# Performance work log

Measured on AMD Instinct MI355X. Metric: run time of the kernel, lower is better.

Reference implementation:

```python
import jax, jax.numpy as jnp
import numpy as np

B, NKV, NQ, D, H = 4, 2048, 1024, 1024, 16
HD = D // H


def setup_inputs() -> dict:
    key = jax.random.key(0)
    ks = jax.random.split(key, 9)
    s = 0.02
    return {
        "x": jax.random.normal(ks[0], (B, NKV, D), jnp.float32),
        "y": jax.random.normal(ks[1], (B, NQ, D), jnp.float32),
        "mask": jax.random.randint(ks[2], (B, NQ, NKV), 0, 2, jnp.int32),
        "W_kv": jax.random.normal(ks[3], (D, 2 * D), jnp.float32) * s,
        "b_kv": jnp.zeros((2 * D,), jnp.float32),
        "W_q": jax.random.normal(ks[4], (D, D), jnp.float32) * s,
        "b_q": jnp.zeros((D,), jnp.float32),
        "W_o": jax.random.normal(ks[5], (D, D), jnp.float32) * s,
        "b_o": jnp.zeros((D,), jnp.float32),
    }


def reference(x, y, mask, W_kv, b_kv, W_q, b_q, W_o, b_o):
    b, nkv, _ = x.shape
    nq = y.shape[1]
    kv = x @ W_kv + b_kv                                  # [B, NKV, 2D]
    q = y @ W_q + b_q                                     # [B, NQ, D]
    kv = kv.reshape(b, nkv, H, 2 * HD).transpose(0, 2, 1, 3)  # [B,H,NKV,2HD]
    q = q.reshape(b, nq, H, HD).transpose(0, 2, 1, 3)         # [B,H,NQ,HD]
    k, v = kv[..., :HD], kv[..., HD:]
    scores = jnp.einsum('bhqd,bhkd->bhqk', q, k) / jnp.sqrt(jnp.float32(HD))
    scores = jnp.where(mask[:, None, :, :] == 0, jnp.float32(-1e20), scores)
    attn = jax.nn.softmax(scores, axis=-1)
    vals = jnp.einsum('bhqk,bhkd->bhqd', attn, v)          # [B,H,NQ,HD]
    vals = vals.transpose(0, 2, 1, 3).reshape(b, nq, D)
    return vals @ W_o + b_o
```

## Files before the change

### kernel.cpp

```cpp
#include <hip/hip_runtime.h>
#include <hip/hip_bf16.h>
#include <math.h>

#define B_   4
#define NKV_ 2048
#define NQ_  1024
#define D_   1024
#define H_   16
#define HD_  64

typedef __attribute__((ext_vector_type(8))) short bf16x8;
typedef __attribute__((ext_vector_type(4))) float f32x4;

#define MFMA16x32(a, b, c) __builtin_amdgcn_mfma_f32_16x16x32_bf16((a), (b), (c), 0, 0, 0)

#define SC_LOG2 0.1803368801111244f

__device__ __forceinline__ short f2bf(float f) {
    unsigned u = __builtin_bit_cast(unsigned, f);
    u = (u + 0x7fff + ((u >> 16) & 1)) >> 16;
    return (short)u;
}
__device__ __forceinline__ unsigned cvt_pk_bf16(float lo, float hi) {
    unsigned r;
    asm("v_cvt_pk_bf16_f32 %0, %1, %2" : "=v"(r) : "v"(lo), "v"(hi));
    return r;
}
__device__ __forceinline__ void gload_lds16(const void* g, void* l) {
    __builtin_amdgcn_global_load_lds(
        (const __attribute__((address_space(1))) void*)g,
        (__attribute__((address_space(3))) void*)l, 16, 0, 0);
}
__device__ __forceinline__ void barrier_raw() {
    asm volatile("" ::: "memory");
    __builtin_amdgcn_s_barrier();
    asm volatile("" ::: "memory");
}

__global__ __launch_bounds__(256)
void prep(const float* __restrict__ Wkv, short* __restrict__ Tkv,
          const float* __restrict__ Wq,  short* __restrict__ Tq,
          const float* __restrict__ Wo,  short* __restrict__ To,
          const int* __restrict__ mask,  unsigned short* __restrict__ m16,
          const float* __restrict__ x,   short* __restrict__ xh, int n4x,
          const float* __restrict__ y,   short* __restrict__ yh, int n4y)
{
    const int bid = (int)blockIdx.x;
    if (bid < 4096) {
        const float* W; short* T; int K, N, bx, by;
        if (bid < 2048)      { W = Wkv; T = Tkv; K = D_; N = 2 * D_; bx = bid & 63;          by = bid >> 6; }
        else if (bid < 3072) { W = Wq;  T = Tq;  K = D_; N = D_;     bx = (bid - 2048) & 31; by = (bid - 2048) >> 5; }
        else                 { W = Wo;  T = To;  K = D_; N = D_;     bx = (bid - 3072) & 31; by = (bid - 3072) >> 5; }
        __shared__ float tile[32][33];
        const int tx = threadIdx.x & 31, ty = threadIdx.x >> 5;
        const int n0 = bx * 32, k0 = by * 32;
#pragma unroll
        for (int i = 0; i < 4; ++i)
            tile[ty + 8 * i][tx] = W[(size_t)(k0 + ty + 8 * i) * N + n0 + tx];
        __syncthreads();
#pragma unroll
        for (int i = 0; i < 4; ++i)
            T[(size_t)(n0 + ty + 8 * i) * K + k0 + tx] = f2bf(tile[tx][ty + 8 * i]);
    } else if (bid < 4608) {
        const int w = (bid - 4096) * 256 + threadIdx.x;
        const int4* pp = reinterpret_cast<const int4*>(mask + (size_t)w * 64);
        unsigned wg0 = 0, wg1 = 0, wg2 = 0, wg3 = 0;
#pragma unroll
        for (int i = 0; i < 16; ++i) {
            const int4 v = pp[i];
            const unsigned nib = (unsigned)(v.x != 0) | ((unsigned)(v.y != 0) << 1)
                               | ((unsigned)(v.z != 0) << 2) | ((unsigned)(v.w != 0) << 3);
            const unsigned sh = 4u * (unsigned)(i >> 2);
            if ((i & 3) == 0) wg0 |= nib << sh;
            else if ((i & 3) == 1) wg1 |= nib << sh;
            else if ((i & 3) == 2) wg2 |= nib << sh;
            else wg3 |= nib << sh;
        }
        ushort4 o;
        o.x = (unsigned short)wg0; o.y = (unsigned short)wg1;
        o.z = (unsigned short)wg2; o.w = (unsigned short)wg3;
        reinterpret_cast<ushort4*>(m16)[w] = o;
    } else {
        const int ntot = n4x + n4y;
        for (int i = (bid - 4608) * 256 + threadIdx.x; i < ntot; i += 2048 * 256) {
            const float4 v = (i < n4x)
                ? reinterpret_cast<const float4*>(x)[i]
                : reinterpret_cast<const float4*>(y)[i - n4x];
            short4 h;
            h.x = f2bf(v.x); h.y = f2bf(v.y); h.z = f2bf(v.z); h.w = f2bf(v.w);
            if (i < n4x) reinterpret_cast<short4*>(xh)[i] = h;
            else         reinterpret_cast<short4*>(yh)[i - n4x] = h;
        }
    }
}

__global__ __launch_bounds__(512, 2)
void proj256(const short* __restrict__ A, const short* __restrict__ Bm,
             const float* __restrict__ bias, short* __restrict__ Kout,
             short* __restrict__ Vtout)
{
    constexpr int K  = 1024;
    constexpr int NT = K / 32;
    constexpr int M  = B_ * NKV_;
    constexpr int N  = 2 * D_;

    __shared__ short At[4][8192];
    __shared__ short Bt[4][8192];

    const int t    = threadIdx.x;
    const int wave = t >> 6;
    const int lane = t & 63;
    const int fr   = lane & 15;
    const int kq   = lane >> 4;
    const int wm0  = (wave >> 2) * 128;
    const int wn0  = (wave & 3) * 64;

    const int gx  = N >> 8;
    const int gy  = M >> 8;
    const int lgx = __builtin_ctz(gx);
    const int bid = (int)blockIdx.x;
    const int xcd = bid & 7;
    const int j   = bid >> 3;
    const int m0  = (xcd * (gy >> 3) + (j >> lgx)) * 256;
    const int n0  = (j & (gx - 1)) * 256;

    const int r1 = t >> 2;
    const int g1 = (t & 3) ^ ((r1 >> 1) & 3);
    const int r2 = r1 + 128;

    f32x4 acc[8][4];
#pragma unroll
    for (int i = 0; i < 8; ++i)
#pragma unroll
        for (int j2 = 0; j2 < 4; ++j2) acc[i][j2] = f32x4{0.f, 0.f, 0.f, 0.f};

    auto stage = [&](int sb, int it) {
        const int kk = it << 5;
        gload_lds16(A  + (size_t)(m0 + r1) * K + kk + 8 * g1, &At[sb][wave * 512]);
        gload_lds16(A  + (size_t)(m0 + r2) * K + kk + 8 * g1, &At[sb][4096 + wave * 512]);
        gload_lds16(Bm + (size_t)(n0 + r1) * K + kk + 8 * g1, &Bt[sb][wave * 512]);
        gload_lds16(Bm + (size_t)(n0 + r2) * K + kk + 8 * g1, &Bt[sb][4096 + wave * 512]);
    };

    stage(0, 0);
    stage(1, 1);
    stage(2, 2);

    const int gsw = ((kq ^ ((fr >> 1) & 3)) << 3);
    for (int it = 0; it < NT; ++it) {
        if (it < NT - 2)       asm volatile("s_waitcnt vmcnt(8)" ::: "memory");
        else if (it == NT - 2) asm volatile("s_waitcnt vmcnt(4)" ::: "memory");
        else                   asm volatile("s_waitcnt vmcnt(0)" ::: "memory");
        barrier_raw();

        const int cb = it & 3;
        bf16x8 af[8], bf[4];
#pragma unroll
        for (int i = 0; i < 8; ++i)
            af[i] = *reinterpret_cast<const bf16x8*>(
                &At[cb][(wm0 + i * 16 + fr) * 32 + gsw]);
#pragma unroll
        for (int i = 0; i < 4; ++i)
            bf[i] = *reinterpret_cast<const bf16x8*>(
                &Bt[cb][(wn0 + i * 16 + fr) * 32 + gsw]);

        if (it + 3 < NT) stage((it + 3) & 3, it + 3);

        __builtin_amdgcn_s_setprio(1);
#pragma unroll
        for (int i = 0; i < 8; ++i)
#pragma unroll
            for (int j2 = 0; j2 < 4; ++j2)
                acc[i][j2] = MFMA16x32(af[i], bf[j2], acc[i][j2]);
        __builtin_amdgcn_s_setprio(0);
    }

#pragma unroll
    for (int i = 0; i < 8; ++i) {
#pragma unroll
        for (int j2 = 0; j2 < 4; ++j2) {
#pragma unroll
            for (int r = 0; r < 4; ++r) {
                const int m = m0 + wm0 + i * 16 + (lane >> 4) * 4 + r;
                const int n = n0 + wn0 + j2 * 16 + fr;
                const float v = acc[i][j2][r] + bias[n];
                const int b  = m >> 11;
                const int nk = m & 2047;
                const int h  = n >> 7;
                const int c  = n & 127;
                const int bh = b * H_ + h;
                if (c < 64)
                    Kout[(((size_t)bh * NKV_ + nk) << 6) + c] = f2bf(v);
                else
                    Vtout[((size_t)bh * 64 + (c - 64)) * NKV_ + nk] = f2bf(v);
            }
        }
    }
}

template<int MODE>
__global__ __launch_bounds__(256)
void gemm64(const short* __restrict__ Ahi, const short* __restrict__ Bhi,
            const float* __restrict__ bias, void* __restrict__ outv)
{
    __shared__ short At[3][2048];
    __shared__ short Bt[3][4096];

    const int M = B_ * NQ_, N = D_, K = D_;
    const int t    = threadIdx.x;
    const int wave = t >> 6;
    const int lane = t & 63;
    const int fr   = lane & 15;
    const int kq   = lane >> 4;

    const int gx  = N >> 7;
    const int gy  = M >> 6;
    const int lgx = __builtin_ctz(gx);
    const int bid = (int)blockIdx.x;
    const int xcd = bid & 7;
    const int j   = bid >> 3;
    const int m0  = (xcd * (gy >> 3) + (j >> lgx)) * 64;
    const int n0  = (j & (gx - 1)) * 128;

    const int wm0 = (wave & 1) * 32;
    const int wn0 = (wave >> 1) * 64;
    const int NT  = K >> 5;

    const int rA = t >> 2, gA = (t & 3) ^ ((rA >> 1) & 3);
    const int r1 = t >> 2,         g1 = (t & 3) ^ ((r1 >> 1) & 3);
    const int r2 = (t + 256) >> 2, g2 = (t & 3) ^ ((r2 >> 1) & 3);

    f32x4 acc[2][4];
#pragma unroll
    for (int i = 0; i < 2; ++i)
#pragma unroll
        for (int j2 = 0; j2 < 4; ++j2) acc[i][j2] = f32x4{0.f, 0.f, 0.f, 0.f};

    auto stage = [&](int sb, int it) {
        const int kk = it << 5;
        gload_lds16(Ahi + (size_t)(m0 + rA) * K + kk + 8 * gA, &At[sb][wave * 512]);
        gload_lds16(Bhi + (size_t)(n0 + r1) * K + kk + 8 * g1, &Bt[sb][wave * 512]);
        gload_lds16(Bhi + (size_t)(n0 + r2) * K + kk + 8 * g2, &Bt[sb][2048 + wave * 512]);
    };

    stage(0, 0);
    if (NT > 1) stage(1, 1);

    const int gsw = ((kq ^ ((fr >> 1) & 3)) << 3);
    for (int it = 0; it < NT; ++it) {
        if (it + 1 < NT) asm volatile("s_waitcnt vmcnt(3)" ::: "memory");
        else             asm volatile("s_waitcnt vmcnt(0)" ::: "memory");
        barrier_raw();

        const int cb = it % 3;
        bf16x8 af[2], bf[4];
#pragma unroll
        for (int i = 0; i < 2; ++i)
            af[i] = *reinterpret_cast<const bf16x8*>(&At[cb][(wm0 + i * 16 + fr) * 32 + gsw]);
#pragma unroll
        for (int i = 0; i < 4; ++i)
            bf[i] = *reinterpret_cast<const bf16x8*>(&Bt[cb][(wn0 + i * 16 + fr) * 32 + gsw]);
        if (it + 2 < NT) stage((it + 2) % 3, it + 2);

        __builtin_amdgcn_s_setprio(1);
#pragma unroll
        for (int i = 0; i < 2; ++i)
#pragma unroll
            for (int j2 = 0; j2 < 4; ++j2)
                acc[i][j2] = MFMA16x32(af[i], bf[j2], acc[i][j2]);
        __builtin_amdgcn_s_setprio(0);
    }

#pragma unroll
    for (int i = 0; i < 2; ++i)
#pragma unroll
        for (int j2 = 0; j2 < 4; ++j2)
#pragma unroll
            for (int r = 0; r < 4; ++r) {
                const int m = m0 + wm0 + i * 16 + (lane >> 4) * 4 + r;
                const int n = n0 + wn0 + j2 * 16 + fr;
                const float v = acc[i][j2][r] + bias[n];
                if (MODE == 1) {
                    short* Q_ = (short*)outv;
                    const int b = m >> 10;
                    const int q = m & 1023;
                    const int h = n >> 6;
                    const int d = n & 63;
                    Q_[(((size_t)(b * H_ + h) * NQ_ + q) << 6) + d] =
                        f2bf(v * SC_LOG2);
                } else {
                    ((float*)outv)[(size_t)m * N + n] = v;
                }
            }
}

__global__ __launch_bounds__(512)
void attn_mfma(const short* __restrict__ Q, const short* __restrict__ K,
               const short* __restrict__ Vt,
               const unsigned short* __restrict__ m16,
               short* __restrict__ valshi)
{
    __shared__ short KtL[3][4096];
    __shared__ short VtL[3][4096];
    __shared__ short PsL[8192];

    const int t    = threadIdx.x;
    const int wave = t >> 6;
    const int lane = t & 63;
    const int fr   = lane & 15;
    const int g    = lane >> 4;

    const int bid = (int)blockIdx.x;
    const int xcd = bid & 7;
    const int j   = bid >> 3;
    const int bh  = xcd * 8 + (j >> 3);
    const int b   = bh >> 4;
    const int h   = bh & 15;
    const int wq0 = (j & 7) * 128 + wave * 16;

    const short* Kg  = K  + (size_t)bh * NKV_ * 64;
    const short* Vtg = Vt + (size_t)bh * 64 * NKV_;

    bf16x8 qf0, qf1;
    {
        const short* Qg = Q + ((size_t)bh * NQ_ + wq0 + fr) * 64 + g * 8;
        qf0 = *reinterpret_cast<const bf16x8*>(Qg);
        qf1 = *reinterpret_cast<const bf16x8*>(Qg + 32);
    }

    bf16x8 ones;
#pragma unroll
    for (int i = 0; i < 8; ++i) ones[i] = (short)0x3F80;

    f32x4 acc_o[4];
#pragma unroll
    for (int n = 0; n < 4; ++n) acc_o[n] = f32x4{0.f, 0.f, 0.f, 0.f};
    f32x4 lacc = f32x4{0.f, 0.f, 0.f, 0.f};

    const unsigned short* mbp =
        m16 + ((size_t)b * NQ_ + wq0 + fr) * (NKV_ / 64) * 4 + g;

    const int r8   = lane >> 3;
    const int csw  = ((lane & 7) << 3) ^ (r8 << 3);
    const int swzf = (fr & 7) << 3;
    short* PsW = PsL + wave * (16 * 64);

    auto stage = [&](int sb, int kt) {
        const short* sK = Kg + (size_t)(kt * 64 + wave * 8 + r8) * 64 + csw;
        gload_lds16(sK, &KtL[sb][(wave * 8) * 64]);
        const short* sV = Vtg + (size_t)(wave * 8 + r8) * NKV_ + kt * 64 + csw;
        gload_lds16(sV, &VtL[sb][(wave * 8) * 64]);
    };

    constexpr int NTK = NKV_ / 64;
    stage(0, 0);
    stage(1, 1);

    const int kcol0 = (8 * g) ^ swzf;
    const int kcol1 = (32 + 8 * g) ^ swzf;

    for (int kt = 0; kt < NTK; ++kt) {
        if (kt + 1 < NTK) asm volatile("s_waitcnt vmcnt(2)" ::: "memory");
        else              asm volatile("s_waitcnt vmcnt(0)" ::: "memory");
        barrier_raw();

        const int cb = kt % 3;
        if (kt + 2 < NTK) stage((kt + 2) % 3, kt + 2);

        const unsigned mskv = mbp[(size_t)kt * 4];

        const short* KB = &KtL[cb][fr * 64];
        f32x4 s_acc[4];
        __builtin_amdgcn_s_setprio(1);
#pragma unroll
        for (int t4 = 0; t4 < 4; ++t4) {
            s_acc[t4] = f32x4{0.f, 0.f, 0.f, 0.f};
            const bf16x8 kf0 = *reinterpret_cast<const bf16x8*>(KB + t4 * 1024 + kcol0);
            const bf16x8 kf1 = *reinterpret_cast<const bf16x8*>(KB + t4 * 1024 + kcol1);
            s_acc[t4] = MFMA16x32(kf0, qf0, s_acc[t4]);
            s_acc[t4] = MFMA16x32(kf1, qf1, s_acc[t4]);
        }
        __builtin_amdgcn_s_setprio(0);

#pragma unroll
        for (int t4 = 0; t4 < 4; ++t4) {
            float e0 = __builtin_amdgcn_exp2f(s_acc[t4][0]);
            float e1 = __builtin_amdgcn_exp2f(s_acc[t4][1]);
            float e2 = __builtin_amdgcn_exp2f(s_acc[t4][2]);
            float e3 = __builtin_amdgcn_exp2f(s_acc[t4][3]);
            e0 = ((mskv >> (4 * t4 + 0)) & 1u) ? e0 : 0.f;
            e1 = ((mskv >> (4 * t4 + 1)) & 1u) ? e1 : 0.f;
            e2 = ((mskv >> (4 * t4 + 2)) & 1u) ? e2 : 0.f;
            e3 = ((mskv >> (4 * t4 + 3)) & 1u) ? e3 : 0.f;
            uint2 w;
            w.x = cvt_pk_bf16(e0, e1);
            w.y = cvt_pk_bf16(e2, e3);
            *reinterpret_cast<uint2*>(&PsW[fr * 64 + ((16 * t4 + 4 * g) ^ swzf)]) = w;
        }

        {
            const bf16x8 pf0 = *reinterpret_cast<const bf16x8*>(&PsW[fr * 64 + kcol0]);
            const bf16x8 pf1 = *reinterpret_cast<const bf16x8*>(&PsW[fr * 64 + kcol1]);
            const short* VB = &VtL[cb][fr * 64];
            __builtin_amdgcn_s_setprio(1);
            lacc = MFMA16x32(ones, pf0, lacc);
            lacc = MFMA16x32(ones, pf1, lacc);
#pragma unroll
            for (int n = 0; n < 4; ++n) {
                const bf16x8 vf0 = *reinterpret_cast<const bf16x8*>(VB + n * 1024 + kcol0);
                const bf16x8 vf1 = *reinterpret_cast<const bf16x8*>(VB + n * 1024 + kcol1);
                acc_o[n] = MFMA16x32(vf0, pf0, acc_o[n]);
                acc_o[n] = MFMA16x32(vf1, pf1, acc_o[n]);
            }
            __builtin_amdgcn_s_setprio(0);
        }
    }

    const float inv = 1.f / lacc[0];
    const size_t obase = ((size_t)b * NQ_ + wq0 + fr) * D_ + h * 64;
#pragma unroll
    for (int n = 0; n < 4; ++n) {
        short4 hh;
        hh.x = f2bf(acc_o[n][0] * inv);
        hh.y = f2bf(acc_o[n][1] * inv);
        hh.z = f2bf(acc_o[n][2] * inv);
        hh.w = f2bf(acc_o[n][3] * inv);
        *reinterpret_cast<short4*>(&valshi[obase + 16 * n + 4 * g]) = hh;
    }
}

extern "C" void kernel_launch(void* const* d_in, const int* in_sizes, int n_in,
                              void* d_out, int out_size, void* d_ws, size_t ws_size,
                              hipStream_t stream)
{
    const float* x    = (const float*)d_in[0];
    const float* y    = (const float*)d_in[1];
    const int*   mask = (const int*)  d_in[2];
    const float* W_kv = (const float*)d_in[3];
    const float* b_kv = (const float*)d_in[4];
    const float* W_q  = (const float*)d_in[5];
    const float* b_q  = (const float*)d_in[6];
    const float* W_o  = (const float*)d_in[7];
    const float* b_o  = (const float*)d_in[8];
    float* out = (float*)d_out;

    char* p = (char*)d_ws;
    auto take = [&](size_t bytes) { char* r = p; p += bytes; return r; };
    short* xhi    = (short*)take((size_t)B_ * NKV_ * D_ * 2);
    short* yhi    = (short*)take((size_t)B_ * NQ_ * D_ * 2);
    short* Wkvthi = (short*)take((size_t)2 * D_ * D_ * 2);
    short* Wqthi  = (short*)take((size_t)D_ * D_ * 2);
    short* Wothi  = (short*)take((size_t)D_ * D_ * 2);
    short* Kbf    = (short*)take((size_t)B_ * H_ * NKV_ * HD_ * 2);
    short* Vtbf   = (short*)take((size_t)B_ * H_ * HD_ * NKV_ * 2);
    short* Qbf    = (short*)take((size_t)B_ * H_ * NQ_ * HD_ * 2);
    unsigned short* m16 =
        (unsigned short*)take((size_t)B_ * NQ_ * (NKV_ / 64) * 4 * 2);
    short* valshi = xhi;

    prep<<<6656, 256, 0, stream>>>(W_kv, Wkvthi, W_q, Wqthi, W_o, Wothi,
                                   mask, m16,
                                   x, xhi, B_ * NKV_ * D_ / 4,
                                   y, yhi, B_ * NQ_ * D_ / 4);

    proj256<<<256, 512, 0, stream>>>(xhi, Wkvthi, b_kv, Kbf, Vtbf);

    gemm64<1><<<512, 256, 0, stream>>>(yhi, Wqthi, b_q, Qbf);

    attn_mfma<<<512, 512, 0, stream>>>(Qbf, Kbf, Vtbf, m16, valshi);

    gemm64<2><<<512, 256, 0, stream>>>(valshi, Wothi, b_o, out);

    (void)in_sizes; (void)n_in; (void)out_size; (void)ws_size;
}
```

Baseline: 162.5 us.

## Software-pipeline attention loop so next tile's QK overlaps current tile's softmax and PV

```diff
diff --git a/kernel.cpp b/kernel.cpp
--- a/kernel.cpp
+++ b/kernel.cpp
@@ -353,41 +353,34 @@
     };
 
     constexpr int NTK = NKV_ / 64;
-    stage(0, 0);
-    stage(1, 1);
-
     const int kcol0 = (8 * g) ^ swzf;
     const int kcol1 = (32 + 8 * g) ^ swzf;
 
-    for (int kt = 0; kt < NTK; ++kt) {
-        if (kt + 1 < NTK) asm volatile("s_waitcnt vmcnt(2)" ::: "memory");
-        else              asm volatile("s_waitcnt vmcnt(0)" ::: "memory");
-        barrier_raw();
-
-        const int cb = kt % 3;
-        if (kt + 2 < NTK) stage((kt + 2) % 3, kt + 2);
-
-        const unsigned mskv = mbp[(size_t)kt * 4];
-
-        const short* KB = &KtL[cb][fr * 64];
-        f32x4 s_acc[4];
+    auto qk = [&](int kt, f32x4 (&s)[4]) {
+        const short* KB = &KtL[kt % 3][fr * 64];
         __builtin_amdgcn_s_setprio(1);
 #pragma unroll
         for (int t4 = 0; t4 < 4; ++t4) {
-            s_acc[t4] = f32x4{0.f, 0.f, 0.f, 0.f};
+            s[t4] = f32x4{0.f, 0.f, 0.f, 0.f};
             const bf16x8 kf0 = *reinterpret_cast<const bf16x8*>(KB + t4 * 1024 + kcol0);
             const bf16x8 kf1 = *reinterpret_cast<const bf16x8*>(KB + t4 * 1024 + kcol1);
-            s_acc[t4] = MFMA16x32(kf0, qf0, s_acc[t4]);
-            s_acc[t4] = MFMA16x32(kf1, qf1, s_acc[t4]);
+            s[t4] = MFMA16x32(kf0, qf0, s[t4]);
+            s[t4] = MFMA16x32(kf1, qf1, s[t4]);
         }
         __builtin_amdgcn_s_setprio(0);
+    };
+
+    auto body = [&](int kt, f32x4 (&sCur)[4], f32x4 (&sNext)[4]) {
+        if (kt + 2 < NTK) stage((kt + 2) % 3, kt + 2);
+
+        const unsigned mskv = mbp[(size_t)kt * 4];
 
 #pragma unroll
         for (int t4 = 0; t4 < 4; ++t4) {
-            float e0 = __builtin_amdgcn_exp2f(s_acc[t4][0]);
-            float e1 = __builtin_amdgcn_exp2f(s_acc[t4][1]);
-            float e2 = __builtin_amdgcn_exp2f(s_acc[t4][2]);
-            float e3 = __builtin_amdgcn_exp2f(s_acc[t4][3]);
+            float e0 = __builtin_amdgcn_exp2f(sCur[t4][0]);
+            float e1 = __builtin_amdgcn_exp2f(sCur[t4][1]);
+            float e2 = __builtin_amdgcn_exp2f(sCur[t4][2]);
+            float e3 = __builtin_amdgcn_exp2f(sCur[t4][3]);
             e0 = ((mskv >> (4 * t4 + 0)) & 1u) ? e0 : 0.f;
             e1 = ((mskv >> (4 * t4 + 1)) & 1u) ? e1 : 0.f;
             e2 = ((mskv >> (4 * t4 + 2)) & 1u) ? e2 : 0.f;
@@ -398,10 +391,12 @@
             *reinterpret_cast<uint2*>(&PsW[fr * 64 + ((16 * t4 + 4 * g) ^ swzf)]) = w;
         }
 
+        if (kt + 1 < NTK) qk(kt + 1, sNext);
+
         {
             const bf16x8 pf0 = *reinterpret_cast<const bf16x8*>(&PsW[fr * 64 + kcol0]);
             const bf16x8 pf1 = *reinterpret_cast<const bf16x8*>(&PsW[fr * 64 + kcol1]);
-            const short* VB = &VtL[cb][fr * 64];
+            const short* VB = &VtL[kt % 3][fr * 64];
             __builtin_amdgcn_s_setprio(1);
             lacc = MFMA16x32(ones, pf0, lacc);
             lacc = MFMA16x32(ones, pf1, lacc);
@@ -414,6 +409,24 @@
             }
             __builtin_amdgcn_s_setprio(0);
         }
+
+        if (kt + 1 < NTK) {
+            asm volatile("s_waitcnt vmcnt(0)" ::: "memory");
+            barrier_raw();
+        }
+    };
+
+    stage(0, 0);
+    stage(1, 1);
+    asm volatile("s_waitcnt vmcnt(0)" ::: "memory");
+    __syncthreads();
+
+    f32x4 sA[4], sB[4];
+    qk(0, sA);
+
+    for (int kt = 0; kt < NTK; kt += 2) {
+        body(kt,     sA, sB);
+        body(kt + 1, sB, sA);
     }
 
     const float inv = 1.f / lacc[0];
```

Result: slower. 188.9 us (+16.3%).
